# Optimization experiments

Hardware: AMD Instinct MI355X
Metric: run time of the kernel (lower is better)

The kernel has to match this reference:

```python
import jax, jax.numpy as jnp
import numpy as np

SCOPE = 63
IN_CHANNELS = 512
DAMP = 0.12
STD = 8.0


def _mexican_hat(scope, damping, std):
    # Ricker wavelet, centered, shape (1, 1, scope)
    x = jnp.arange(scope, dtype=jnp.float32) - (scope - 1) / 2.0
    norm = damping * (2.0 / (jnp.sqrt(3.0 * std) * np.pi ** 0.25))
    k = norm * (1.0 - (x / std) ** 2) * jnp.exp(-(x ** 2) / (2.0 * std ** 2))
    return k[None, None, :]


def setup_inputs() -> dict:
    key = jax.random.key(0)
    activations = jax.random.normal(key, (32, IN_CHANNELS, 56, 56), dtype=jnp.float32)
    inhibition_filter = _mexican_hat(SCOPE, DAMP, STD)
    return {"activations": activations, "inhibition_filter": inhibition_filter}


def _pad_roll(k, in_channels, scope):
    # zero-pad filter to length in_channels, then roll center to index 0 side
    pad_left = (in_channels - scope) // 2
    pad_right = in_channels - scope - pad_left
    padded = jnp.concatenate(
        [jnp.zeros((pad_left,), k.dtype), k, jnp.zeros((pad_right,), k.dtype)]
    )
    return jnp.roll(padded, in_channels // 2 + 1)


def reference(activations, inhibition_filter):
    C = activations.shape[1]
    kernel = _pad_roll(inhibition_filter[0, 0], C, SCOPE)  # (C,)
    # Circulant Toeplitz matrix: tpl[i] = roll(kernel, i), i.e. tpl[i, j] = kernel[(j - i) % C]
    idx = (jnp.arange(C)[None, :] - jnp.arange(C)[:, None]) % C
    tpl = kernel[idx]  # (C, C)
    # Original: [B, HW, C] @ [C, C] contracting input channel (first tpl axis)
    return jnp.einsum('bchw,cd->bdhw', activations, tpl)
```

## Files before the change

### kernel.cpp

```cpp
#include <hip/hip_runtime.h>
#include <hip/hip_bf16.h>
#include <cstddef>


#define NC    512
#define HW    3136
#define NT    32
#define NTILE 98
#define NB    32
#define TPB   256
#define TPW   2
#define NPAIR (NTILE / TPW)

typedef __attribute__((ext_vector_type(8)))  short bf16x8;
typedef __attribute__((ext_vector_type(4)))  float f32x4;
typedef __attribute__((ext_vector_type(16))) float f32x16;

__device__ __forceinline__ short f2bf(float f) {
    union { __hip_bfloat16 h; short s; } u;
    u.h = __float2bfloat16(f);
    return u.s;
}

__device__ __forceinline__ int swzf(int hw) {
    return (((hw & 7) ^ (hw >> 3)) << 4);
}

__device__ __forceinline__ void load_tile(const float* __restrict__ gb,
                                          int wv, int g, int q, f32x4 (&r)[16]) {
    #pragma unroll
    for (int j = 0; j < 8; ++j) {
        const int r0 = wv * 128 + j * 16 + 2 * g;
        r[2 * j]     = *reinterpret_cast<const f32x4*>(gb + (size_t)r0 * HW + 4 * q);
        r[2 * j + 1] = *reinterpret_cast<const f32x4*>(gb + (size_t)(r0 + 1) * HW + 4 * q);
    }
}

__device__ __forceinline__ void store_tile(unsigned short* __restrict__ dst,
                                           int wv, int g, int q, const f32x4 (&r)[16]) {
    #pragma unroll
    for (int j = 0; j < 8; ++j) {
        const int r0 = wv * 128 + j * 16 + 2 * g;
        #pragma unroll
        for (int t4 = 0; t4 < 4; ++t4) {
            const int hw = 4 * q + t4;
            const unsigned int pk = (unsigned int)(unsigned short)f2bf(r[2 * j][t4])
                                  | ((unsigned int)(unsigned short)f2bf(r[2 * j + 1][t4]) << 16);
            const int byte = hw * (NC * 2) + ((r0 * 2) ^ swzf(hw));
            *reinterpret_cast<unsigned int*>(reinterpret_cast<char*>(dst) + byte) = pk;
        }
    }
}

__global__ __launch_bounds__(TPB, 2)
void toeplitz_pipe_kernel(const float* __restrict__ act,
                          const float* __restrict__ filt,
                          float* __restrict__ out) {
    __shared__ __align__(16) unsigned short xs[2][NT * NC];

    const int tid = threadIdx.x;
    const int wv  = tid >> 6;
    const int ln  = tid & 63;
    const int bx  = blockIdx.x;
    const int b   = bx / NPAIR;
    const int pr  = bx - b * NPAIR;
    const int t0  = pr * TPW;

    const int r_a = ln & 31;
    const int k0  = (ln >> 5) * 8;
    bf16x8 af[6];
    #pragma unroll
    for (int m = 0; m < 6; ++m) {
        const int delta = 32 - 16 * m;
        #pragma unroll
        for (int i = 0; i < 8; ++i) {
            const int t = delta + 31 + r_a - (k0 + i);
            af[m][i] = (t >= 0 && t < 63) ? f2bf(filt[t]) : (short)0;
        }
    }

    const int g = ln >> 3;
    const int q = ln & 7;
    const float* gbase = act + (size_t)b * NC * HW;

    {
        f32x4 R[16];
        load_tile(gbase + (size_t)t0 * NT, wv, g, q, R);
        store_tile(xs[0], wv, g, q, R);
    }
    __syncthreads();

    const int hwl     = ln & 31;
    const int rowbyte = hwl * (NC * 2);
    const int swzv    = swzf(hwl);
    const int kbv     = (ln >> 5) * 16;
    const int rhalf   = (ln >> 5) * 4;
    const int cbase   = wv * 128 - 32;

    #pragma unroll
    for (int i = 0; i < TPW; ++i) {
        f32x4 Rn[16];
        if (i + 1 < TPW)
            load_tile(gbase + (size_t)(t0 + i + 1) * NT, wv, g, q, Rn);

        const char* xb = reinterpret_cast<const char*>(xs[i & 1]);
        bf16x8 w[12];
        #pragma unroll
        for (int u = 0; u < 12; ++u) {
            const int c0 = (cbase + 16 * u) & (NC - 1);
            w[u] = *reinterpret_cast<const bf16x8*>(xb + rowbyte + (((c0 * 2) + kbv) ^ swzv));
        }
        float* ob = out + (size_t)b * NC * HW + (size_t)(t0 + i) * NT + hwl;
        #pragma unroll
        for (int j = 0; j < 4; ++j) {
            const int d0 = wv * 128 + j * 32;
            f32x16 acc;
            #pragma unroll
            for (int r = 0; r < 16; ++r) acc[r] = 0.0f;
            #pragma unroll
            for (int m = 0; m < 6; ++m)
                acc = __builtin_amdgcn_mfma_f32_32x32x16_bf16(af[m], w[2 * j + m], acc, 0, 0, 0);
            #pragma unroll
            for (int r = 0; r < 16; ++r) {
                const int row = d0 + (r & 3) + 8 * (r >> 2) + rhalf;
                __builtin_nontemporal_store(acc[r], ob + (size_t)row * HW);
            }
        }

        if (i + 1 < TPW) {
            store_tile(xs[(i + 1) & 1], wv, g, q, Rn);
            __syncthreads();
        }
    }
}

extern "C" void kernel_launch(void* const* d_in, const int* in_sizes, int n_in,
                              void* d_out, int out_size, void* d_ws, size_t ws_size,
                              hipStream_t stream) {
    const float* act  = (const float*)d_in[0];
    const float* filt = (const float*)d_in[1];
    float* out = (float*)d_out;
    dim3 grid(NB * NPAIR);
    dim3 block(TPB);
    hipLaunchKernelGGL(toeplitz_pipe_kernel, grid, block, 0, stream,
                       act, filt, out);
}
```

Measured before the change: 71.91 us.

## Convert to persistent grid-stride kernel with single LDS buffer and register prefetch

Replaces the fixed two-tiles-per-block launch with a persistent grid of 1024 blocks that stride over all batch×tile work items. The next tile is prefetched into registers while the current tile is computed. A single LDS buffer now replaces the double buffer, and launch bounds are raised to allow four blocks per CU. This aims to cut the per-block setup cost (filter fragment build) and the tail imbalance, at the price of an extra barrier per iteration and uneven tile counts per block (3136 tiles over 1024 blocks).

Result: slower. 147.7 us (+105.4%).

```diff
diff --git a/kernel.cpp b/kernel.cpp
--- a/kernel.cpp
+++ b/kernel.cpp
@@ -9,8 +9,8 @@
 #define NTILE 98
 #define NB    32
 #define TPB   256
-#define TPW   2
-#define NPAIR (NTILE / TPW)
+#define GRID  1024
+#define TOTT  (NB * NTILE)
 
 typedef __attribute__((ext_vector_type(8)))  short bf16x8;
 typedef __attribute__((ext_vector_type(4)))  float f32x4;
@@ -52,19 +52,16 @@
     }
 }
 
-__global__ __launch_bounds__(TPB, 2)
-void toeplitz_pipe_kernel(const float* __restrict__ act,
-                          const float* __restrict__ filt,
-                          float* __restrict__ out) {
-    __shared__ __align__(16) unsigned short xs[2][NT * NC];
+__global__ __launch_bounds__(TPB, 4)
+void toeplitz_persist_kernel(const float* __restrict__ act,
+                             const float* __restrict__ filt,
+                             float* __restrict__ out) {
+    __shared__ __align__(16) unsigned short xs[NT * NC];
 
     const int tid = threadIdx.x;
     const int wv  = tid >> 6;
     const int ln  = tid & 63;
     const int bx  = blockIdx.x;
-    const int b   = bx / NPAIR;
-    const int pr  = bx - b * NPAIR;
-    const int t0  = pr * TPW;
 
     const int r_a = ln & 31;
     const int k0  = (ln >> 5) * 8;
@@ -81,14 +78,6 @@
 
     const int g = ln >> 3;
     const int q = ln & 7;
-    const float* gbase = act + (size_t)b * NC * HW;
-
-    {
-        f32x4 R[16];
-        load_tile(gbase + (size_t)t0 * NT, wv, g, q, R);
-        store_tile(xs[0], wv, g, q, R);
-    }
-    __syncthreads();
 
     const int hwl     = ln & 31;
     const int rowbyte = hwl * (NC * 2);
@@ -97,20 +86,35 @@
     const int rhalf   = (ln >> 5) * 4;
     const int cbase   = wv * 128 - 32;
 
-    #pragma unroll
-    for (int i = 0; i < TPW; ++i) {
-        f32x4 Rn[16];
-        if (i + 1 < TPW)
-            load_tile(gbase + (size_t)(t0 + i + 1) * NT, wv, g, q, Rn);
+    f32x4 R[16];
+    {
+        const int b  = bx / NTILE;
+        const int pr = bx - b * NTILE;
+        load_tile(act + (size_t)b * NC * HW + (size_t)pr * NT, wv, g, q, R);
+        store_tile(xs, wv, g, q, R);
+    }
+    __syncthreads();
 
-        const char* xb = reinterpret_cast<const char*>(xs[i & 1]);
+    for (int t = bx; t < TOTT; t += GRID) {
+        const int tn = t + GRID;
+        const bool has_next = tn < TOTT;
+
+        if (has_next) {
+            const int bn  = tn / NTILE;
+            const int prn = tn - bn * NTILE;
+            load_tile(act + (size_t)bn * NC * HW + (size_t)prn * NT, wv, g, q, R);
+        }
+
+        const int b  = t / NTILE;
+        const int pr = t - b * NTILE;
         bf16x8 w[12];
         #pragma unroll
         for (int u = 0; u < 12; ++u) {
             const int c0 = (cbase + 16 * u) & (NC - 1);
-            w[u] = *reinterpret_cast<const bf16x8*>(xb + rowbyte + (((c0 * 2) + kbv) ^ swzv));
+            w[u] = *reinterpret_cast<const bf16x8*>(
+                reinterpret_cast<const char*>(xs) + rowbyte + (((c0 * 2) + kbv) ^ swzv));
         }
-        float* ob = out + (size_t)b * NC * HW + (size_t)(t0 + i) * NT + hwl;
+        float* ob = out + (size_t)b * NC * HW + (size_t)pr * NT + hwl;
         #pragma unroll
         for (int j = 0; j < 4; ++j) {
             const int d0 = wv * 128 + j * 32;
@@ -127,8 +131,9 @@
             }
         }
 
-        if (i + 1 < TPW) {
-            store_tile(xs[(i + 1) & 1], wv, g, q, Rn);
+        __syncthreads();
+        if (has_next) {
+            store_tile(xs, wv, g, q, R);
             __syncthreads();
         }
     }
@@ -140,8 +145,8 @@
     const float* act  = (const float*)d_in[0];
     const float* filt = (const float*)d_in[1];
     float* out = (float*)d_out;
-    dim3 grid(NB * NPAIR);
+    dim3 grid(GRID);
     dim3 block(TPB);
-    hipLaunchKernelGGL(toeplitz_pipe_kernel, grid, block, 0, stream,
+    hipLaunchKernelGGL(toeplitz_persist_kernel, grid, block, 0, stream,
                        act, filt, out);
 }
```
